# Kernel tuning notes

Hardware: AMD Instinct MI355X
Metric: run time of the kernel (lower is better)

The kernel has to match this reference:

```python
import jax, jax.numpy as jnp
import numpy as np

HEADS = 8
DIM_HEAD = 32
SCALE = DIM_HEAD ** -0.5


def setup_inputs() -> dict:
    key = jax.random.key(0)
    ks = jax.random.split(key, 5)
    b, c, H, W = 4, 256, 48, 48
    n = H * W
    hidden = HEADS * DIM_HEAD
    x = jax.random.normal(ks[0], (b, c, H, W), dtype=jnp.float32)
    pos_bias = jax.random.normal(ks[1], (HEADS, n, n), dtype=jnp.float32) * 0.02
    w_qkv = jax.random.normal(ks[2], (hidden * 3, c), dtype=jnp.float32) * (c ** -0.5)
    w_out = jax.random.normal(ks[3], (c, hidden), dtype=jnp.float32) * (hidden ** -0.5)
    b_out = jax.random.normal(ks[4], (c,), dtype=jnp.float32) * 0.01
    return {"x": x, "pos_bias": pos_bias, "w_qkv": w_qkv, "w_out": w_out, "b_out": b_out}


def reference(x, pos_bias, w_qkv, w_out, b_out):
    b, c, H, W = x.shape
    n = H * W
    xf = x.reshape(b, c, n)                                  # [b, c, n]
    qkv = jnp.einsum('oc,bcn->bon', w_qkv, xf)               # 1x1 conv, no bias
    q, k, v = jnp.split(qkv, 3, axis=1)                      # each [b, hidden, n]
    def to_heads(t):
        return t.reshape(b, HEADS, DIM_HEAD, n)              # b h d n
    q, k, v = to_heads(q) * SCALE, to_heads(k), to_heads(v)
    sim = jnp.einsum('bhdi,bhdj->bhij', q, k)                # [b, h, n, n]
    sim = sim + pos_bias[None]                               # broadcast over batch
    attn = jax.nn.softmax(sim, axis=-1)
    out = jnp.einsum('bhij,bhdj->bhid', attn, v)             # [b, h, n, d]
    out = out.transpose(0, 1, 3, 2).reshape(b, HEADS * DIM_HEAD, n)  # b (h d) n
    out = jnp.einsum('oc,bcn->bon', w_out, out) + b_out[None, :, None]
    return out.reshape(b, c, H, W)
```

## Files before the change

### kernel.cpp

```cpp
#include <hip/hip_runtime.h>
#include <stdint.h>
#include <stddef.h>

#define BB 4
#define CC 256
#define NH 8
#define DH 32
#define NN 2304
#define O3 768
#define HID 256
#define QK_SCALE 0.17677669529663687f
#define LOG2E 1.44269504f

typedef __attribute__((ext_vector_type(8))) short short8;
typedef __attribute__((ext_vector_type(4))) float float4v;

__device__ __forceinline__ unsigned short f2bf(float f) {
    union { float f; uint32_t u; } v; v.f = f;
    uint32_t u = v.u;
    return (unsigned short)((u + 0x7FFFu + ((u >> 16) & 1u)) >> 16);
}
__device__ __forceinline__ float bf2f(unsigned short s) {
    union { uint32_t u; float f; } v; v.u = ((uint32_t)s) << 16;
    return v.f;
}

__global__ __launch_bounds__(256) void prep_kernel(const float* __restrict__ x,
                                                   const float* __restrict__ wqkv,
                                                   const float* __restrict__ wout,
                                                   unsigned short* __restrict__ xT,
                                                   unsigned short* __restrict__ whi,
                                                   unsigned short* __restrict__ wlo,
                                                   unsigned short* __restrict__ wob) {
    const int bid = blockIdx.x;
    const int t = threadIdx.x;
    if (bid < 2304) {
        const int n0 = (bid % 72) * 32, c0 = ((bid / 72) % 8) * 32, b = bid / 576;
        __shared__ float ls[32][33];
        {
            int c = t >> 3, nc = (t & 7) * 4;
            float4 v4 = *(const float4*)(x + ((size_t)b * CC + c0 + c) * NN + n0 + nc);
            ls[c][nc] = v4.x; ls[c][nc + 1] = v4.y; ls[c][nc + 2] = v4.z; ls[c][nc + 3] = v4.w;
        }
        __syncthreads();
        {
            int n = t >> 3, cl = (t & 7) * 4;
            uint32_t p0 = (uint32_t)f2bf(ls[cl + 0][n]) | ((uint32_t)f2bf(ls[cl + 1][n]) << 16);
            uint32_t p1 = (uint32_t)f2bf(ls[cl + 2][n]) | ((uint32_t)f2bf(ls[cl + 3][n]) << 16);
            uint32_t* dst = (uint32_t*)(xT + ((size_t)b * NN + n0 + n) * CC + c0 + cl);
            dst[0] = p0; dst[1] = p1;
        }
    } else {
        int i = (bid - 2304) * 256 + t;
        float wv = wqkv[i];
        unsigned short hi = f2bf(wv);
        whi[i] = hi;
        wlo[i] = f2bf(wv - bf2f(hi));
        if (i < HID * HID) wob[i] = f2bf(wout[i]);
    }
}

__global__ __launch_bounds__(256) void qkv_gemm_bf16(const unsigned short* __restrict__ xT,
                                                     const unsigned short* __restrict__ whi,
                                                     const unsigned short* __restrict__ wlo,
                                                     unsigned short* __restrict__ q,
                                                     unsigned short* __restrict__ k,
                                                     unsigned short* __restrict__ v) {
    const int og = blockIdx.x;
    const int n0 = blockIdx.y * 64;
    const int b  = blockIdx.z;
    const int t = threadIdx.x;
    const int w = t >> 6, lane = t & 63, l15 = lane & 15, quad = lane >> 4;
    const unsigned short* xb = xT + (size_t)b * NN * CC;

    float4v acc[4] = {{0.f,0.f,0.f,0.f},{0.f,0.f,0.f,0.f},
                      {0.f,0.f,0.f,0.f},{0.f,0.f,0.f,0.f}};

    if (og < 8) {
        const int o0 = og * 64;
        const unsigned short* ap = xb + (size_t)(n0 + w * 16 + l15) * CC + quad * 8;
        #pragma unroll
        for (int c0 = 0; c0 < CC; c0 += 32) {
            short8 af = *(const short8*)(ap + c0);
            #pragma unroll
            for (int jj = 0; jj < 4; ++jj) {
                const size_t wo = (size_t)(o0 + jj * 16 + l15) * CC + c0 + quad * 8;
                short8 bh = *(const short8*)(whi + wo);
                short8 bl = *(const short8*)(wlo + wo);
                acc[jj] = __builtin_amdgcn_mfma_f32_16x16x32_bf16(af, bh, acc[jj], 0, 0, 0);
                acc[jj] = __builtin_amdgcn_mfma_f32_16x16x32_bf16(af, bl, acc[jj], 0, 0, 0);
            }
        }
        #pragma unroll
        for (int jj = 0; jj < 4; ++jj) {
            const int o = o0 + jj * 16 + l15;
            const int which = o >> 8;
            const int h = (o >> 5) & 7, d = o & 31;
            unsigned short* dst = which ? k : q;
            const float sc = which ? 1.0f : QK_SCALE * LOG2E;
            #pragma unroll
            for (int r = 0; r < 4; ++r) {
                const int n = n0 + w * 16 + quad * 4 + r;
                dst[(((size_t)b * NH + h) * NN + n) * DH + d] = f2bf(acc[jj][r] * sc);
            }
        }
    } else {
        const int o0 = 512 + (og - 8) * 64;
        const size_t wr = (size_t)(o0 + w * 16 + l15) * CC + quad * 8;
        #pragma unroll
        for (int c0 = 0; c0 < CC; c0 += 32) {
            short8 ah = *(const short8*)(whi + wr + c0);
            short8 al = *(const short8*)(wlo + wr + c0);
            #pragma unroll
            for (int jj = 0; jj < 4; ++jj) {
                short8 bf = *(const short8*)(xb + (size_t)(n0 + jj * 16 + l15) * CC + c0 + quad * 8);
                acc[jj] = __builtin_amdgcn_mfma_f32_16x16x32_bf16(ah, bf, acc[jj], 0, 0, 0);
                acc[jj] = __builtin_amdgcn_mfma_f32_16x16x32_bf16(al, bf, acc[jj], 0, 0, 0);
            }
        }
        #pragma unroll
        for (int r = 0; r < 4; ++r) {
            const int o = o0 + w * 16 + quad * 4 + r;
            const int h = (o >> 5) & 7, d = o & 31;
            #pragma unroll
            for (int jj = 0; jj < 4; ++jj) {
                const int n = n0 + jj * 16 + l15;
                v[(((size_t)b * NH + h) * DH + d) * NN + n] = f2bf(acc[jj][r]);
            }
        }
    }
}

__device__ __forceinline__ void bias_store(float (*bc)[36], int qr, int kc, float4 v) {
    const int Lb = (qr >> 2) * 16;
    const int iq = qr & 3;
    const int kh = (kc >> 4) * 4 + iq;
    const int kl = kc & 15;
    bc[Lb + kl + 0][kh] = v.x * LOG2E;
    bc[Lb + kl + 1][kh] = v.y * LOG2E;
    bc[Lb + kl + 2][kh] = v.z * LOG2E;
    bc[Lb + kl + 3][kh] = v.w * LOG2E;
}

__global__ __launch_bounds__(256) void attn_kernel(const unsigned short* __restrict__ qg,
                                                   const unsigned short* __restrict__ kg,
                                                   const unsigned short* __restrict__ vg,
                                                   const float* __restrict__ bias,
                                                   unsigned short* __restrict__ ao) {
    const int i0   = blockIdx.x * 16;
    const int h    = blockIdx.y;
    const int t    = threadIdx.x;
    const int b    = t >> 6;
    const int lane = t & 63;
    const int l15  = lane & 15;
    const int quad = lane >> 4;

    __shared__ __align__(16) float bias_c[2][64][36];
    __shared__ __align__(16) unsigned short ps[BB][16][136];

    const size_t bh = (size_t)b * NH + h;
    const unsigned short* qp = qg + bh * NN * DH;
    const unsigned short* kp = kg + bh * NN * DH;
    const unsigned short* vp = vg + bh * DH * NN;

    short8 qf = *(const short8*)(qp + (size_t)(i0 + l15) * DH + quad * 8);

    float4v oa0 = {0.f, 0.f, 0.f, 0.f};
    float4v oa1 = {0.f, 0.f, 0.f, 0.f};
    float l_r[4] = {0.f, 0.f, 0.f, 0.f};

    const float* bsrc = bias + ((size_t)h * NN + i0) * NN;
    const int srow = t >> 5;
    const int scol = (t & 31) * 4;

    {
        float4 a = *(const float4*)(bsrc + (size_t)srow * NN + scol);
        float4 c = *(const float4*)(bsrc + (size_t)(srow + 8) * NN + scol);
        bias_store(bias_c[0], srow, scol, a);
        bias_store(bias_c[0], srow + 8, scol, c);
    }
    short8 ka[8], kb[8];
    #pragma unroll
    for (int jj = 0; jj < 8; ++jj)
        ka[jj] = *(const short8*)(kp + (size_t)(jj * 16 + l15) * DH + quad * 8);
    __syncthreads();

#define ATTN_PHASE(KC, KN, JT, PJT, HAVEP, CUR, NXT)                               \
{                                                                                  \
                             \
    short8 vv[8];                                                                  \
    _Pragma("unroll")                                                              \
    for (int cc = 0; cc < 4; ++cc) {                                               \
        vv[2*cc]   = *(const short8*)(vp + (size_t)l15 * NN + (JT) + cc*32 + quad*8);        \
        vv[2*cc+1] = *(const short8*)(vp + (size_t)(l15+16) * NN + (JT) + cc*32 + quad*8);   \
    }                                                                              \
                           \
    if (HAVEP) {                                                                   \
        _Pragma("unroll")                                                          \
        for (int jj = 0; jj < 8; ++jj)                                             \
            KN[jj] = *(const short8*)(kp + (size_t)((PJT) + jj*16 + l15) * DH + quad*8);     \
    }                                                                              \
                           \
    float4 bga, bgc;                                                               \
    if (HAVEP) {                                                                   \
        bga = *(const float4*)(bsrc + (size_t)srow * NN + (PJT) + scol);           \
        bgc = *(const float4*)(bsrc + (size_t)(srow + 8) * NN + (PJT) + scol);     \
    }                                                                              \
                  \
    float4v s[8];                                                                  \
    _Pragma("unroll")                                                              \
    for (int jj = 0; jj < 8; ++jj) {                                               \
        float4v bfr = *(const float4v*)&bias_c[CUR][quad * 16 + l15][jj * 4];      \
        s[jj] = __builtin_amdgcn_mfma_f32_16x16x32_bf16(qf, KC[jj], bfr, 0, 0, 0); \
    }                                                                              \
           \
    _Pragma("unroll")                                                              \
    for (int r = 0; r < 4; ++r) {                                                  \
        const int row = quad * 4 + r;                                              \
        float pv_[8];                                                              \
        _Pragma("unroll")                                                          \
        for (int jj = 0; jj < 8; ++jj) { pv_[jj] = exp2f(s[jj][r]); l_r[r] += pv_[jj]; }     \
        _Pragma("unroll")                                                          \
        for (int jp = 0; jp < 4; ++jp) {                                           \
            uint32_t pk;                                                           \
            asm("v_cvt_pk_bf16_f32 %0, %1, %2" : "=v"(pk) : "v"(pv_[2*jp]), "v"(pv_[2*jp+1])); \
            ps[b][row][(2*jp) * 16 + l15]     = (unsigned short)pk;                \
            ps[b][row][(2*jp+1) * 16 + l15]   = (unsigned short)(pk >> 16);        \
        }                                                                          \
    }                                                                              \
              \
    _Pragma("unroll")                                                              \
    for (int cc = 0; cc < 4; ++cc) {                                               \
        short8 pa = *(const short8*)&ps[b][l15][cc * 32 + quad * 8];               \
        oa0 = __builtin_amdgcn_mfma_f32_16x16x32_bf16(pa, vv[2*cc],   oa0, 0, 0, 0);         \
        oa1 = __builtin_amdgcn_mfma_f32_16x16x32_bf16(pa, vv[2*cc+1], oa1, 0, 0, 0);         \
    }                                                                              \
           \
    if (HAVEP) {                                                                   \
        bias_store(bias_c[NXT], srow, scol, bga);                                  \
        bias_store(bias_c[NXT], srow + 8, scol, bgc);                              \
    }                                                                              \
    __syncthreads();                                                               \
}

    for (int jt0 = 0; jt0 < NN; jt0 += 256) {
        ATTN_PHASE(ka, kb, jt0,       jt0 + 128, true,               0, 1)
        ATTN_PHASE(kb, ka, jt0 + 128, jt0 + 256, (jt0 + 256 < NN),   1, 0)
    }
#undef ATTN_PHASE

    #pragma unroll
    for (int r = 0; r < 4; ++r) {
        #pragma unroll
        for (int off = 1; off < 16; off <<= 1)
            l_r[r] += __shfl_xor(l_r[r], off, 64);
    }

    unsigned short* aop = ao + ((size_t)b * NN + i0) * HID + h * DH;
    #pragma unroll
    for (int r = 0; r < 4; ++r) {
        const int row = quad * 4 + r;
        const float inv = 1.0f / l_r[r];
        aop[(size_t)row * HID + l15]      = f2bf(oa0[r] * inv);
        aop[(size_t)row * HID + 16 + l15] = f2bf(oa1[r] * inv);
    }
}

__global__ __launch_bounds__(256) void out_proj(const unsigned short* __restrict__ wob,
                                                const unsigned short* __restrict__ aob,
                                                const float* __restrict__ bout,
                                                float* __restrict__ out) {
    const int n0 = blockIdx.x * 64;
    const int o0 = blockIdx.y * 64;
    const int b  = blockIdx.z;
    const int t = threadIdx.x;
    const int w = t >> 6, lane = t & 63, l15 = lane & 15, quad = lane >> 4;
    const int orow = o0 + w * 16;

    float4v acc[4] = {{0.f,0.f,0.f,0.f},{0.f,0.f,0.f,0.f},
                      {0.f,0.f,0.f,0.f},{0.f,0.f,0.f,0.f}};
    const unsigned short* ap = aob + ((size_t)b * NN + n0) * HID;
    #pragma unroll
    for (int c0 = 0; c0 < HID; c0 += 32) {
        short8 af = *(const short8*)(wob + (size_t)(orow + l15) * HID + c0 + quad * 8);
        #pragma unroll
        for (int jj = 0; jj < 4; ++jj) {
            short8 bf = *(const short8*)(ap + (size_t)(jj * 16 + l15) * HID + c0 + quad * 8);
            acc[jj] = __builtin_amdgcn_mfma_f32_16x16x32_bf16(af, bf, acc[jj], 0, 0, 0);
        }
    }
    float* op = out + (size_t)b * HID * NN;
    #pragma unroll
    for (int r = 0; r < 4; ++r) {
        const int o = orow + quad * 4 + r;
        const float bv = bout[o];
        #pragma unroll
        for (int jj = 0; jj < 4; ++jj)
            op[(size_t)o * NN + n0 + jj * 16 + l15] = acc[jj][r] + bv;
    }
}

extern "C" void kernel_launch(void* const* d_in, const int* in_sizes, int n_in,
                              void* d_out, int out_size, void* d_ws, size_t ws_size,
                              hipStream_t stream) {
    const float* x        = (const float*)d_in[0];
    const float* pos_bias = (const float*)d_in[1];
    const float* w_qkv    = (const float*)d_in[2];
    const float* w_out    = (const float*)d_in[3];
    const float* b_out    = (const float*)d_in[4];
    float* out = (float*)d_out;

    char* ws = (char*)d_ws;
    unsigned short* q   = (unsigned short*)(ws);
    unsigned short* k   = (unsigned short*)(ws + 4718592);
    unsigned short* v   = (unsigned short*)(ws + 9437184);
    unsigned short* ao  = (unsigned short*)(ws + 14155776);
    unsigned short* wob = (unsigned short*)(ws + 18874368);
    unsigned short* whi = (unsigned short*)(ws + 19005440);
    unsigned short* wlo = (unsigned short*)(ws + 19398656);
    unsigned short* xT  = (unsigned short*)(ws + 19791872);

    prep_kernel<<<3072, 256, 0, stream>>>(x, w_qkv, w_out, xT, whi, wlo, wob);
    qkv_gemm_bf16<<<dim3(12, NN / 64, BB), 256, 0, stream>>>(xT, whi, wlo, q, k, v);
    attn_kernel<<<dim3(NN / 16, NH), 256, 0, stream>>>(q, k, v, pos_bias, ao);
    out_proj<<<dim3(NN / 64, HID / 64, BB), 256, 0, stream>>>(wob, ao, b_out, out);
}
```

Before: 430.5 us.

## Load position bias directly into registers and drop LDS staging and barriers

The attention kernel no longer stages the position-bias tile through a double-buffered shared-memory array with block-wide barriers. Each lane now loads its own bias elements straight from global memory into register double buffers, and K fragments are loaded at the start of each phase instead of being prefetched a phase ahead. This removes the LDS transpose writes and the per-phase __syncthreads, at the cost of scalar, less coalesced bias loads (4-byte loads strided by 16 columns), more registers, and less K prefetch overlap.

```diff
diff --git a/kernel.cpp b/kernel.cpp
--- a/kernel.cpp
+++ b/kernel.cpp
@@ -131,17 +131,6 @@
     }
 }
 
-__device__ __forceinline__ void bias_store(float (*bc)[36], int qr, int kc, float4 v) {
-    const int Lb = (qr >> 2) * 16;
-    const int iq = qr & 3;
-    const int kh = (kc >> 4) * 4 + iq;
-    const int kl = kc & 15;
-    bc[Lb + kl + 0][kh] = v.x * LOG2E;
-    bc[Lb + kl + 1][kh] = v.y * LOG2E;
-    bc[Lb + kl + 2][kh] = v.z * LOG2E;
-    bc[Lb + kl + 3][kh] = v.w * LOG2E;
-}
-
 __global__ __launch_bounds__(256) void attn_kernel(const unsigned short* __restrict__ qg,
                                                    const unsigned short* __restrict__ kg,
                                                    const unsigned short* __restrict__ vg,
@@ -155,8 +144,7 @@
     const int l15  = lane & 15;
     const int quad = lane >> 4;
 
-    __shared__ __align__(16) float bias_c[2][64][36];
-    __shared__ __align__(16) unsigned short ps[BB][16][136];
+    __shared__ unsigned short ps[BB][16][136];
 
     const size_t bh = (size_t)b * NH + h;
     const unsigned short* qp = qg + bh * NN * DH;
@@ -169,83 +157,72 @@
     float4v oa1 = {0.f, 0.f, 0.f, 0.f};
     float l_r[4] = {0.f, 0.f, 0.f, 0.f};
 
-    const float* bsrc = bias + ((size_t)h * NN + i0) * NN;
-    const int srow = t >> 5;
-    const int scol = (t & 31) * 4;
-
-    {
-        float4 a = *(const float4*)(bsrc + (size_t)srow * NN + scol);
-        float4 c = *(const float4*)(bsrc + (size_t)(srow + 8) * NN + scol);
-        bias_store(bias_c[0], srow, scol, a);
-        bias_store(bias_c[0], srow + 8, scol, c);
-    }
-    short8 ka[8], kb[8];
-    #pragma unroll
-    for (int jj = 0; jj < 8; ++jj)
-        ka[jj] = *(const short8*)(kp + (size_t)(jj * 16 + l15) * DH + quad * 8);
-    __syncthreads();
-
-#define ATTN_PHASE(KC, KN, JT, PJT, HAVEP, CUR, NXT)                               \
+    const float* bp = bias + ((size_t)h * NN + i0 + quad * 4) * NN + l15;
+
+    float ba[32], bb[32];
+    #pragma unroll
+    for (int r = 0; r < 4; ++r)
+        #pragma unroll
+        for (int jj = 0; jj < 8; ++jj)
+            ba[r * 8 + jj] = bp[(size_t)r * NN + jj * 16];
+
+#define ATTN_PHASE(BC, BN, JT, PJT, HAVEP)                                         \
 {                                                                                  \
-                             \
+            \
+    short8 kf[8];                                                                  \
+    _Pragma("unroll")                                                              \
+    for (int jj = 0; jj < 8; ++jj)                                                 \
+        kf[jj] = *(const short8*)(kp + (size_t)((JT) + jj * 16 + l15) * DH + quad * 8); \
+                                \
     short8 vv[8];                                                                  \
     _Pragma("unroll")                                                              \
     for (int cc = 0; cc < 4; ++cc) {                                               \
-        vv[2*cc]   = *(const short8*)(vp + (size_t)l15 * NN + (JT) + cc*32 + quad*8);        \
-        vv[2*cc+1] = *(const short8*)(vp + (size_t)(l15+16) * NN + (JT) + cc*32 + quad*8);   \
-    }                                                                              \
-                           \
+        vv[2*cc]   = *(const short8*)(vp + (size_t)l15 * NN      + (JT) + cc*32 + quad*8); \
+        vv[2*cc+1] = *(const short8*)(vp + (size_t)(l15+16) * NN + (JT) + cc*32 + quad*8); \
+    }                                                                              \
+               \
     if (HAVEP) {                                                                   \
         _Pragma("unroll")                                                          \
-        for (int jj = 0; jj < 8; ++jj)                                             \
-            KN[jj] = *(const short8*)(kp + (size_t)((PJT) + jj*16 + l15) * DH + quad*8);     \
-    }                                                                              \
-                           \
-    float4 bga, bgc;                                                               \
-    if (HAVEP) {                                                                   \
-        bga = *(const float4*)(bsrc + (size_t)srow * NN + (PJT) + scol);           \
-        bgc = *(const float4*)(bsrc + (size_t)(srow + 8) * NN + (PJT) + scol);     \
-    }                                                                              \
-                  \
+        for (int r = 0; r < 4; ++r)                                                \
+            _Pragma("unroll")                                                      \
+            for (int jj = 0; jj < 8; ++jj)                                         \
+                BN[r * 8 + jj] = bp[(size_t)r * NN + (PJT) + jj * 16];             \
+    }                                                                              \
+            \
     float4v s[8];                                                                  \
     _Pragma("unroll")                                                              \
     for (int jj = 0; jj < 8; ++jj) {                                               \
-        float4v bfr = *(const float4v*)&bias_c[CUR][quad * 16 + l15][jj * 4];      \
-        s[jj] = __builtin_amdgcn_mfma_f32_16x16x32_bf16(qf, KC[jj], bfr, 0, 0, 0); \
-    }                                                                              \
-           \
+        float4v ci = { BC[0*8+jj] * LOG2E, BC[1*8+jj] * LOG2E,                     \
+                       BC[2*8+jj] * LOG2E, BC[3*8+jj] * LOG2E };                   \
+        s[jj] = __builtin_amdgcn_mfma_f32_16x16x32_bf16(qf, kf[jj], ci, 0, 0, 0);  \
+    }                                                                              \
+             \
     _Pragma("unroll")                                                              \
     for (int r = 0; r < 4; ++r) {                                                  \
         const int row = quad * 4 + r;                                              \
         float pv_[8];                                                              \
         _Pragma("unroll")                                                          \
-        for (int jj = 0; jj < 8; ++jj) { pv_[jj] = exp2f(s[jj][r]); l_r[r] += pv_[jj]; }     \
+        for (int jj = 0; jj < 8; ++jj) { pv_[jj] = exp2f(s[jj][r]); l_r[r] += pv_[jj]; } \
         _Pragma("unroll")                                                          \
         for (int jp = 0; jp < 4; ++jp) {                                           \
             uint32_t pk;                                                           \
             asm("v_cvt_pk_bf16_f32 %0, %1, %2" : "=v"(pk) : "v"(pv_[2*jp]), "v"(pv_[2*jp+1])); \
-            ps[b][row][(2*jp) * 16 + l15]     = (unsigned short)pk;                \
-            ps[b][row][(2*jp+1) * 16 + l15]   = (unsigned short)(pk >> 16);        \
+            ps[b][row][(2*jp)   * 16 + l15] = (unsigned short)pk;                  \
+            ps[b][row][(2*jp+1) * 16 + l15] = (unsigned short)(pk >> 16);          \
         }                                                                          \
     }                                                                              \
               \
     _Pragma("unroll")                                                              \
     for (int cc = 0; cc < 4; ++cc) {                                               \
         short8 pa = *(const short8*)&ps[b][l15][cc * 32 + quad * 8];               \
-        oa0 = __builtin_amdgcn_mfma_f32_16x16x32_bf16(pa, vv[2*cc],   oa0, 0, 0, 0);         \
-        oa1 = __builtin_amdgcn_mfma_f32_16x16x32_bf16(pa, vv[2*cc+1], oa1, 0, 0, 0);         \
-    }                                                                              \
-           \
-    if (HAVEP) {                                                                   \
-        bias_store(bias_c[NXT], srow, scol, bga);                                  \
-        bias_store(bias_c[NXT], srow + 8, scol, bgc);                              \
-    }                                                                              \
-    __syncthreads();                                                               \
+        oa0 = __builtin_amdgcn_mfma_f32_16x16x32_bf16(pa, vv[2*cc],   oa0, 0, 0, 0); \
+        oa1 = __builtin_amdgcn_mfma_f32_16x16x32_bf16(pa, vv[2*cc+1], oa1, 0, 0, 0); \
+    }                                                                              \
 }
 
     for (int jt0 = 0; jt0 < NN; jt0 += 256) {
-        ATTN_PHASE(ka, kb, jt0,       jt0 + 128, true,               0, 1)
-        ATTN_PHASE(kb, ka, jt0 + 128, jt0 + 256, (jt0 + 256 < NN),   1, 0)
+        ATTN_PHASE(ba, bb, jt0,       jt0 + 128, true)
+        ATTN_PHASE(bb, ba, jt0 + 128, jt0 + 256, (jt0 + 256 < NN))
     }
 #undef ATTN_PHASE
 
```

Measured after the change: 435.1 us. No clear change (+1.1%).
